# Kernel tuning notes

Hardware: AMD Instinct MI355X
Metric: run time of the kernel (lower is better)

Reference implementation:

```python
import jax, jax.numpy as jnp
import numpy as np

D_MODEL = 1024
N_HEADS = 16
D_HEAD = D_MODEL // N_HEADS
WINDOW = 256
SCALE = D_HEAD ** -0.5


def setup_inputs() -> dict:
    key = jax.random.key(0)
    k1, k2, k3, k4, k5 = jax.random.split(key, 5)
    B, S = 2, 2048
    x = jax.random.normal(k1, (B, S, D_MODEL), dtype=jnp.float32)
    s = 0.02
    Wqkv = jax.random.normal(k2, (D_MODEL, 3 * D_MODEL), dtype=jnp.float32) * s
    bqkv = jnp.zeros((3 * D_MODEL,), dtype=jnp.float32)
    Wout = jax.random.normal(k3, (D_MODEL, D_MODEL), dtype=jnp.float32) * s
    bout = jnp.zeros((D_MODEL,), dtype=jnp.float32)
    return {"x": x, "Wqkv": Wqkv, "bqkv": bqkv, "Wout": Wout, "bout": bout}


def reference(x, Wqkv, bqkv, Wout, bout):
    B, S, D = x.shape
    qkv = x @ Wqkv + bqkv                       # (B, S, 3D)
    q, k, v = jnp.split(qkv, 3, axis=-1)
    # (B, H, S, d)
    q = q.reshape(B, S, N_HEADS, D_HEAD).transpose(0, 2, 1, 3)
    k = k.reshape(B, S, N_HEADS, D_HEAD).transpose(0, 2, 1, 3)
    v = v.reshape(B, S, N_HEADS, D_HEAD).transpose(0, 2, 1, 3)
    scores = jnp.einsum('bhqd,bhkd->bhqk', q, k) * SCALE
    # windowed causal mask: allow j <= i and j >= i - WINDOW (inclusive),
    # matching torch code where mask[i, :i-window_size] = 0 for i >= window_size
    i = jnp.arange(S)[:, None]
    j = jnp.arange(S)[None, :]
    allowed = (j <= i) & (j >= i - WINDOW)      # (S, S)
    scores = jnp.where(allowed[None, None], scores, -jnp.inf)
    attn = jax.nn.softmax(scores, axis=-1)      # dropout=0 / eval mode
    out = jnp.einsum('bhqk,bhkd->bhqd', attn, v)
    out = out.transpose(0, 2, 1, 3).reshape(B, S, D)
    return out @ Wout + bout
```

## Files before the change

kernel.cpp:

```cpp
#include <hip/hip_runtime.h>
#include <stdint.h>


typedef __attribute__((ext_vector_type(8))) short bf16x8;
typedef __attribute__((ext_vector_type(4))) float f32x4;
typedef __attribute__((ext_vector_type(4))) unsigned int u32x4;
typedef __attribute__((ext_vector_type(4))) unsigned short u16x4;

#define DEV static __device__ __forceinline__

#define SC2 0.18033688011112042f

DEV unsigned short f2bf(float f) {
  unsigned int u = __builtin_bit_cast(unsigned int, f);
  u += 0x7fffu + ((u >> 16) & 1u);
  return (unsigned short)(u >> 16);
}

DEV void gload_lds16(const void* g, void* l) {
  __builtin_amdgcn_global_load_lds((const __attribute__((address_space(1))) void*)g,
                                   (__attribute__((address_space(3))) void*)l,
                                   16, 0, 0);
}

__global__ __launch_bounds__(256) void k_prep(const float* __restrict__ x,
                                              const float* __restrict__ Wqkv,
                                              const float* __restrict__ Wout,
                                              const float* __restrict__ bqkv,
                                              unsigned short* __restrict__ xb,
                                              unsigned short* __restrict__ wqT,
                                              unsigned short* __restrict__ woT,
                                              float* __restrict__ bqkv_s) {
  __shared__ float t[32][33];
  const int bid = blockIdx.x, tid = threadIdx.x;
  if (bid < 4096) {
    int i = bid * 256 + tid;
    f32x4 v = ((const f32x4*)x)[i];
    u16x4 o;
    o[0] = f2bf(v[0]); o[1] = f2bf(v[1]); o[2] = f2bf(v[2]); o[3] = f2bf(v[3]);
    ((u16x4*)xb)[i] = o;
    return;
  }
  if (bid >= 8192) {
    int i = (bid - 8192) * 256 + tid;
    if (i < 3072) bqkv_s[i] = bqkv[i] * (i < 1024 ? SC2 : 1.0f);
    return;
  }
  const float* in;
  unsigned short* out;
  int N, K, n0, k0;
  float wscale = 1.0f;
  if (bid < 7168) {
    int tt = bid - 4096;
    in = Wqkv; out = wqT; N = 3072; K = 1024;
    n0 = (tt % 96) * 32; k0 = (tt / 96) * 32;
    if (n0 < 1024) wscale = SC2;
  } else {
    int tt = bid - 7168;
    in = Wout; out = woT; N = 1024; K = 1024;
    n0 = (tt % 32) * 32; k0 = (tt / 32) * 32;
  }
  const int tx = tid & 31, ty = tid >> 5;
#pragma unroll
  for (int i = 0; i < 4; ++i)
    t[ty + i * 8][tx] = in[(size_t)(k0 + ty + i * 8) * N + n0 + tx];
  __syncthreads();
#pragma unroll
  for (int i = 0; i < 4; ++i)
    out[(size_t)(n0 + ty + i * 8) * K + k0 + tx] = f2bf(t[tx][ty + i * 8] * wscale);
}

template <int BN, bool F32OUT, bool FUSE_VT>
__global__ __launch_bounds__(512) void k_gemmbig(const unsigned short* __restrict__ A,
                                                 const unsigned short* __restrict__ Bt,
                                                 const float* __restrict__ bias,
                                                 void* __restrict__ Cout,
                                                 unsigned short* __restrict__ vT,
                                                 int M, int N, int K) {
  constexpr int NI = BN / 32;
  constexpr int ACH = 32;
  constexpr int NCH = ACH + BN / 8;
  constexpr int ASZ = 256 * 64;
  constexpr int BSZ = BN * 64;
  extern __shared__ unsigned short lds[];
  const int tid = threadIdx.x;
  const int lane = tid & 63, wid = tid >> 6;
  const int wr = wid >> 1, wc = wid & 1;
  const int g = lane >> 4, li = lane & 15;
  const int m0 = blockIdx.y * 256, n0 = blockIdx.x * BN;

  f32x4 acc[4][NI] = {};
  const int nkt = K >> 6;
  const int r8 = lane >> 3, sp = lane & 7;

  auto Abuf = [&](int i) { return lds + i * ASZ; };
  auto Bbuf = [&](int i) { return lds + 2 * ASZ + i * BSZ; };

  auto stage = [&](int bufi, int kt) {
#pragma unroll
    for (int c = wid; c < NCH; c += 8) {
      if (c < ACH) {
        int row = c * 8 + r8;
        int sl = sp ^ (row & 7);
        gload_lds16(A + (size_t)(m0 + row) * K + kt * 64 + sl * 8,
                    Abuf(bufi) + c * 512);
      } else {
        int cc = c - ACH;
        int row = cc * 8 + r8;
        int sl = sp ^ (row & 7);
        gload_lds16(Bt + (size_t)(n0 + row) * K + kt * 64 + sl * 8,
                    Bbuf(bufi) + cc * 512);
      }
    }
  };

  stage(0, 0);
  for (int kt = 0; kt < nkt; ++kt) {
    __syncthreads();
    if (kt + 1 < nkt) stage((kt + 1) & 1, kt + 1);
    const unsigned short* Ac = Abuf(kt & 1);
    const unsigned short* Bc = Bbuf(kt & 1);
#pragma unroll
    for (int h = 0; h < 2; ++h) {
      bf16x8 af[4], bfr[NI];
#pragma unroll
      for (int mi = 0; mi < 4; ++mi) {
        const int r = wr * 64 + mi * 16 + li;
        const int slot = (g + h * 4) ^ (r & 7);
        af[mi] = *(const bf16x8*)&Ac[r * 64 + slot * 8];
      }
#pragma unroll
      for (int ni = 0; ni < NI; ++ni) {
        const int r = wc * (BN / 2) + ni * 16 + li;
        const int slot = (g + h * 4) ^ (r & 7);
        bfr[ni] = *(const bf16x8*)&Bc[r * 64 + slot * 8];
      }
#pragma unroll
      for (int mi = 0; mi < 4; ++mi)
#pragma unroll
        for (int ni = 0; ni < NI; ++ni)
          acc[mi][ni] = __builtin_amdgcn_mfma_f32_16x16x32_bf16(af[mi], bfr[ni],
                                                                acc[mi][ni], 0, 0, 0);
    }
  }

  float bv[NI];
#pragma unroll
  for (int ni = 0; ni < NI; ++ni) bv[ni] = bias[n0 + wc * (BN / 2) + ni * 16 + li];
#pragma unroll
  for (int mi = 0; mi < 4; ++mi) {
#pragma unroll
    for (int ni = 0; ni < NI; ++ni) {
      const int col = n0 + wc * (BN / 2) + ni * 16 + li;
      const int row0 = m0 + wr * 64 + mi * 16 + g * 4;
      float v0 = acc[mi][ni][0] + bv[ni];
      float v1 = acc[mi][ni][1] + bv[ni];
      float v2 = acc[mi][ni][2] + bv[ni];
      float v3 = acc[mi][ni][3] + bv[ni];
      if (F32OUT) {
        float* C = (float*)Cout;
        C[(size_t)(row0 + 0) * N + col] = v0;
        C[(size_t)(row0 + 1) * N + col] = v1;
        C[(size_t)(row0 + 2) * N + col] = v2;
        C[(size_t)(row0 + 3) * N + col] = v3;
      } else {
        unsigned short* C = (unsigned short*)Cout;
        C[(size_t)(row0 + 0) * N + col] = f2bf(v0);
        C[(size_t)(row0 + 1) * N + col] = f2bf(v1);
        C[(size_t)(row0 + 2) * N + col] = f2bf(v2);
        C[(size_t)(row0 + 3) * N + col] = f2bf(v3);
      }
      if (FUSE_VT && col >= 2048) {
        const int b = row0 >> 11;
        const int s = row0 & 2047;
        u16x4 vv;
        vv[0] = f2bf(v0); vv[1] = f2bf(v1); vv[2] = f2bf(v2); vv[3] = f2bf(v3);
        *(u16x4*)&vT[(size_t)(b * 1024 + col - 2048) * 2048 + s] = vv;
      }
    }
  }
}

__global__ __launch_bounds__(256) void k_attn3(const unsigned short* __restrict__ qkv,
                                               const unsigned short* __restrict__ vT,
                                               unsigned short* __restrict__ attn) {
  __shared__ unsigned short Ks[2][64 * 64];
  __shared__ unsigned short Vs[2][64 * 64];
  __shared__ unsigned short Ps[64 * 88];
  const int tid = threadIdx.x, lane = tid & 63, wid = tid >> 6;
  const int g = lane >> 4, li = lane & 15;
  const int bh = blockIdx.y, b = bh >> 4, h = bh & 15;
  const int q0 = blockIdx.x * 64;
  const size_t rs = 3072;
  const unsigned short* qb = qkv + (size_t)b * 2048 * rs + h * 64;
  const unsigned short* kb = qb + 1024;
  const unsigned short* vb = vT + (size_t)bh * 64 * 2048;

  const int qrow = wid * 16 + li;
  const bf16x8 qf0 = *(const bf16x8*)(qb + (size_t)(q0 + qrow) * rs + (g << 3));
  const bf16x8 qf1 = *(const bf16x8*)(qb + (size_t)(q0 + qrow) * rs + 32 + (g << 3));

  const int tf = (blockIdx.x >= 4) ? 0 : (4 - (int)blockIdx.x);

  auto stage = [&](int bufi, int t) {
    const int j0 = q0 - 256 + t * 64;
    const int sl = (lane & 7) ^ ((lane >> 3) & 7);
#pragma unroll
    for (int j = 0; j < 2; ++j) {
      const int chunk = wid * 2 + j;
      const int row = chunk * 8 + (lane >> 3);
      gload_lds16(kb + (size_t)(j0 + row) * rs + sl * 8, &Ks[bufi][chunk * 512]);
      gload_lds16(vb + (size_t)row * 2048 + j0 + sl * 8, &Vs[bufi][chunk * 512]);
    }
  };

  f32x4 o[4] = {};
  float l_part[4] = {0.f, 0.f, 0.f, 0.f};

  stage(0, tf);
  int cur = 0;
  for (int t = tf; t < 5; ++t) {
    if (t + 1 < 5) {
      stage(cur ^ 1, t + 1);
      asm volatile("s_waitcnt vmcnt(4)" ::: "memory");
    } else {
      asm volatile("s_waitcnt vmcnt(0)" ::: "memory");
    }
    __builtin_amdgcn_sched_barrier(0);
    __builtin_amdgcn_s_barrier();
    __builtin_amdgcn_sched_barrier(0);

    const unsigned short* Kc = Ks[cur];
    const unsigned short* Vc = Vs[cur];

    f32x4 s[4];
#pragma unroll
    for (int ni = 0; ni < 4; ++ni) {
      const int kr = ni * 16 + li;
      const int sw = (kr & 7);
      bf16x8 kf0 = *(const bf16x8*)&Kc[kr * 64 + ((g ^ sw) << 3)];
      bf16x8 kf1 = *(const bf16x8*)&Kc[kr * 64 + (((4 + g) ^ sw) << 3)];
      f32x4 z = {};
      z = __builtin_amdgcn_mfma_f32_16x16x32_bf16(qf0, kf0, z, 0, 0, 0);
      z = __builtin_amdgcn_mfma_f32_16x16x32_bf16(qf1, kf1, z, 0, 0, 0);
      s[ni] = z;
    }
    const int rt = wid * 16 + g * 4;
#pragma unroll
    for (int ni = 0; ni < 4; ++ni) {
      int ct = ni * 16 + li;
#pragma unroll
      for (int reg = 0; reg < 4; ++reg) {
        float sv = s[ni][reg];
        if (t == 4 && ct > rt + reg) sv = -3e30f;
        if (t == 0 && ct < rt + reg) sv = -3e30f;
        s[ni][reg] = sv;
      }
    }
#pragma unroll
    for (int reg = 0; reg < 4; ++reg) {
      float ps = 0.f;
#pragma unroll
      for (int ni = 0; ni < 4; ++ni) {
        float p = __builtin_exp2f(s[ni][reg] - 16.0f);
        ps += p;
        Ps[(wid * 16 + g * 4 + reg) * 88 + ni * 16 + li] = f2bf(p);
      }
      l_part[reg] += ps;
    }
    asm volatile("s_waitcnt lgkmcnt(0)" ::: "memory");
    __builtin_amdgcn_sched_barrier(0);
    const bf16x8 pf0 = *(const bf16x8*)&Ps[(wid * 16 + li) * 88 + (g << 3)];
    const bf16x8 pf1 = *(const bf16x8*)&Ps[(wid * 16 + li) * 88 + 32 + (g << 3)];
#pragma unroll
    for (int ni = 0; ni < 4; ++ni) {
      const int dr = ni * 16 + li;
      const int sw = (dr & 7);
      bf16x8 vf0 = *(const bf16x8*)&Vc[dr * 64 + ((g ^ sw) << 3)];
      bf16x8 vf1 = *(const bf16x8*)&Vc[dr * 64 + (((4 + g) ^ sw) << 3)];
      o[ni] = __builtin_amdgcn_mfma_f32_16x16x32_bf16(pf0, vf0, o[ni], 0, 0, 0);
      o[ni] = __builtin_amdgcn_mfma_f32_16x16x32_bf16(pf1, vf1, o[ni], 0, 0, 0);
    }
    __builtin_amdgcn_sched_barrier(0);
    __builtin_amdgcn_s_barrier();
    cur ^= 1;
  }

  float inv[4];
#pragma unroll
  for (int reg = 0; reg < 4; ++reg) {
    float L = l_part[reg];
    L += __shfl_xor(L, 1, 64);
    L += __shfl_xor(L, 2, 64);
    L += __shfl_xor(L, 4, 64);
    L += __shfl_xor(L, 8, 64);
    inv[reg] = 1.f / L;
  }
#pragma unroll
  for (int ni = 0; ni < 4; ++ni) {
#pragma unroll
    for (int reg = 0; reg < 4; ++reg) {
      size_t row = (size_t)b * 2048 + q0 + wid * 16 + g * 4 + reg;
      attn[row * 1024 + h * 64 + ni * 16 + li] = f2bf(o[ni][reg] * inv[reg]);
    }
  }
}

extern "C" void kernel_launch(void* const* d_in, const int* in_sizes, int n_in,
                              void* d_out, int out_size, void* d_ws, size_t ws_size,
                              hipStream_t stream) {
  const float* x    = (const float*)d_in[0];
  const float* Wqkv = (const float*)d_in[1];
  const float* bqkv = (const float*)d_in[2];
  const float* Wout = (const float*)d_in[3];
  const float* bout = (const float*)d_in[4];
  float* out = (float*)d_out;

  uint8_t* ws = (uint8_t*)d_ws;
  unsigned short* xb    = (unsigned short*)(ws);
  unsigned short* wqT   = (unsigned short*)(ws +  8388608);
  unsigned short* woT   = (unsigned short*)(ws + 14680064);
  unsigned short* qkvb  = (unsigned short*)(ws + 16777216);
  unsigned short* attnb = (unsigned short*)(ws + 41943040);
  unsigned short* vTb   = (unsigned short*)(ws + 50331648);
  float*          bqs   = (float*)(ws + 58720256);

  hipFuncSetAttribute((const void*)k_gemmbig<192, false, true>,
                      hipFuncAttributeMaxDynamicSharedMemorySize, 114688);
  hipFuncSetAttribute((const void*)k_gemmbig<64, true, false>,
                      hipFuncAttributeMaxDynamicSharedMemorySize, 81920);

  k_prep<<<8204, 256, 0, stream>>>(x, Wqkv, Wout, bqkv, xb, wqT, woT, bqs);
  k_gemmbig<192, false, true><<<dim3(3072 / 192, 4096 / 256), 512, 114688, stream>>>(
      xb, wqT, bqs, qkvb, vTb, 4096, 3072, 1024);
  k_attn3<<<dim3(2048 / 64, 32), 256, 0, stream>>>(qkvb, vTb, attnb);
  k_gemmbig<64, true, false><<<dim3(1024 / 64, 4096 / 256), 512, 81920, stream>>>(
      attnb, woT, bout, out, nullptr, 4096, 1024, 1024);
}
```

Measured before the change: 85.73 us.

## Double attention query tile to 128 rows with 8 waves sharing K/V tiles

The windowed attention kernel now handles 128 query rows per block with 512 threads. The two 4-wave halves share each staged 64-row K/V tile, and each half skips the one tile outside its window. This roughly cuts K/V global loads and staging per query row while giving each thread fewer staging loads. The cost is half the number of blocks, an extra tile iteration per block where some waves idle at barriers, and a larger LDS footprint for P.

```diff
diff --git a/kernel.cpp b/kernel.cpp
--- a/kernel.cpp
+++ b/kernel.cpp
@@ -181,16 +181,16 @@
   }
 }
 
-__global__ __launch_bounds__(256) void k_attn3(const unsigned short* __restrict__ qkv,
+__global__ __launch_bounds__(512) void k_attn5(const unsigned short* __restrict__ qkv,
                                                const unsigned short* __restrict__ vT,
                                                unsigned short* __restrict__ attn) {
   __shared__ unsigned short Ks[2][64 * 64];
   __shared__ unsigned short Vs[2][64 * 64];
-  __shared__ unsigned short Ps[64 * 88];
+  __shared__ unsigned short Ps[128 * 88];
   const int tid = threadIdx.x, lane = tid & 63, wid = tid >> 6;
   const int g = lane >> 4, li = lane & 15;
   const int bh = blockIdx.y, b = bh >> 4, h = bh & 15;
-  const int q0 = blockIdx.x * 64;
+  const int bx = blockIdx.x, q0 = bx * 128;
   const size_t rs = 3072;
   const unsigned short* qb = qkv + (size_t)b * 2048 * rs + h * 64;
   const unsigned short* kb = qb + 1024;
@@ -200,29 +200,27 @@
   const bf16x8 qf0 = *(const bf16x8*)(qb + (size_t)(q0 + qrow) * rs + (g << 3));
   const bf16x8 qf1 = *(const bf16x8*)(qb + (size_t)(q0 + qrow) * rs + 32 + (g << 3));
 
-  const int tf = (blockIdx.x >= 4) ? 0 : (4 - (int)blockIdx.x);
+  const int tf_blk = (bx >= 2) ? 0 : (4 - 2 * bx);
+  const int tfw = (wid >= 4) ? 1 : 0;
+  const int tlw = tfw + 4;
 
   auto stage = [&](int bufi, int t) {
     const int j0 = q0 - 256 + t * 64;
-    const int sl = (lane & 7) ^ ((lane >> 3) & 7);
-#pragma unroll
-    for (int j = 0; j < 2; ++j) {
-      const int chunk = wid * 2 + j;
-      const int row = chunk * 8 + (lane >> 3);
-      gload_lds16(kb + (size_t)(j0 + row) * rs + sl * 8, &Ks[bufi][chunk * 512]);
-      gload_lds16(vb + (size_t)row * 2048 + j0 + sl * 8, &Vs[bufi][chunk * 512]);
-    }
+    const int row = wid * 8 + (lane >> 3);
+    const int sl = (lane & 7) ^ (row & 7);
+    gload_lds16(kb + (size_t)(j0 + row) * rs + sl * 8, &Ks[bufi][wid * 512]);
+    gload_lds16(vb + (size_t)row * 2048 + j0 + sl * 8, &Vs[bufi][wid * 512]);
   };
 
   f32x4 o[4] = {};
   float l_part[4] = {0.f, 0.f, 0.f, 0.f};
 
-  stage(0, tf);
+  stage(0, tf_blk);
   int cur = 0;
-  for (int t = tf; t < 5; ++t) {
-    if (t + 1 < 5) {
+  for (int t = tf_blk; t < 6; ++t) {
+    if (t + 1 < 6) {
       stage(cur ^ 1, t + 1);
-      asm volatile("s_waitcnt vmcnt(4)" ::: "memory");
+      asm volatile("s_waitcnt vmcnt(2)" ::: "memory");
     } else {
       asm volatile("s_waitcnt vmcnt(0)" ::: "memory");
     }
@@ -230,56 +228,58 @@
     __builtin_amdgcn_s_barrier();
     __builtin_amdgcn_sched_barrier(0);
 
-    const unsigned short* Kc = Ks[cur];
-    const unsigned short* Vc = Vs[cur];
-
-    f32x4 s[4];
-#pragma unroll
-    for (int ni = 0; ni < 4; ++ni) {
-      const int kr = ni * 16 + li;
-      const int sw = (kr & 7);
-      bf16x8 kf0 = *(const bf16x8*)&Kc[kr * 64 + ((g ^ sw) << 3)];
-      bf16x8 kf1 = *(const bf16x8*)&Kc[kr * 64 + (((4 + g) ^ sw) << 3)];
-      f32x4 z = {};
-      z = __builtin_amdgcn_mfma_f32_16x16x32_bf16(qf0, kf0, z, 0, 0, 0);
-      z = __builtin_amdgcn_mfma_f32_16x16x32_bf16(qf1, kf1, z, 0, 0, 0);
-      s[ni] = z;
-    }
-    const int rt = wid * 16 + g * 4;
-#pragma unroll
-    for (int ni = 0; ni < 4; ++ni) {
-      int ct = ni * 16 + li;
+    if (t >= tfw && t <= tlw) {
+      const unsigned short* Kc = Ks[cur];
+      const unsigned short* Vc = Vs[cur];
+
+      f32x4 s[4];
+#pragma unroll
+      for (int ni = 0; ni < 4; ++ni) {
+        const int kr = ni * 16 + li;
+        const int sw = (kr & 7);
+        bf16x8 kf0 = *(const bf16x8*)&Kc[kr * 64 + ((g ^ sw) << 3)];
+        bf16x8 kf1 = *(const bf16x8*)&Kc[kr * 64 + (((4 + g) ^ sw) << 3)];
+        f32x4 z = {};
+        z = __builtin_amdgcn_mfma_f32_16x16x32_bf16(qf0, kf0, z, 0, 0, 0);
+        z = __builtin_amdgcn_mfma_f32_16x16x32_bf16(qf1, kf1, z, 0, 0, 0);
+        s[ni] = z;
+      }
+      const int rt = (wid & 3) * 16 + g * 4;
+#pragma unroll
+      for (int ni = 0; ni < 4; ++ni) {
+        int ct = ni * 16 + li;
+#pragma unroll
+        for (int reg = 0; reg < 4; ++reg) {
+          float sv = s[ni][reg];
+          if (t == tlw && ct > rt + reg) sv = -3e30f;
+          if (t == tfw && ct < rt + reg) sv = -3e30f;
+          s[ni][reg] = sv;
+        }
+      }
 #pragma unroll
       for (int reg = 0; reg < 4; ++reg) {
-        float sv = s[ni][reg];
-        if (t == 4 && ct > rt + reg) sv = -3e30f;
-        if (t == 0 && ct < rt + reg) sv = -3e30f;
-        s[ni][reg] = sv;
-      }
-    }
-#pragma unroll
-    for (int reg = 0; reg < 4; ++reg) {
-      float ps = 0.f;
+        float ps = 0.f;
+#pragma unroll
+        for (int ni = 0; ni < 4; ++ni) {
+          float p = __builtin_exp2f(s[ni][reg] - 16.0f);
+          ps += p;
+          Ps[(wid * 16 + g * 4 + reg) * 88 + ni * 16 + li] = f2bf(p);
+        }
+        l_part[reg] += ps;
+      }
+      asm volatile("s_waitcnt lgkmcnt(0)" ::: "memory");
+      __builtin_amdgcn_sched_barrier(0);
+      const bf16x8 pf0 = *(const bf16x8*)&Ps[(wid * 16 + li) * 88 + (g << 3)];
+      const bf16x8 pf1 = *(const bf16x8*)&Ps[(wid * 16 + li) * 88 + 32 + (g << 3)];
 #pragma unroll
       for (int ni = 0; ni < 4; ++ni) {
-        float p = __builtin_exp2f(s[ni][reg] - 16.0f);
-        ps += p;
-        Ps[(wid * 16 + g * 4 + reg) * 88 + ni * 16 + li] = f2bf(p);
-      }
-      l_part[reg] += ps;
-    }
-    asm volatile("s_waitcnt lgkmcnt(0)" ::: "memory");
-    __builtin_amdgcn_sched_barrier(0);
-    const bf16x8 pf0 = *(const bf16x8*)&Ps[(wid * 16 + li) * 88 + (g << 3)];
-    const bf16x8 pf1 = *(const bf16x8*)&Ps[(wid * 16 + li) * 88 + 32 + (g << 3)];
-#pragma unroll
-    for (int ni = 0; ni < 4; ++ni) {
-      const int dr = ni * 16 + li;
-      const int sw = (dr & 7);
-      bf16x8 vf0 = *(const bf16x8*)&Vc[dr * 64 + ((g ^ sw) << 3)];
-      bf16x8 vf1 = *(const bf16x8*)&Vc[dr * 64 + (((4 + g) ^ sw) << 3)];
-      o[ni] = __builtin_amdgcn_mfma_f32_16x16x32_bf16(pf0, vf0, o[ni], 0, 0, 0);
-      o[ni] = __builtin_amdgcn_mfma_f32_16x16x32_bf16(pf1, vf1, o[ni], 0, 0, 0);
+        const int dr = ni * 16 + li;
+        const int sw = (dr & 7);
+        bf16x8 vf0 = *(const bf16x8*)&Vc[dr * 64 + ((g ^ sw) << 3)];
+        bf16x8 vf1 = *(const bf16x8*)&Vc[dr * 64 + (((4 + g) ^ sw) << 3)];
+        o[ni] = __builtin_amdgcn_mfma_f32_16x16x32_bf16(pf0, vf0, o[ni], 0, 0, 0);
+        o[ni] = __builtin_amdgcn_mfma_f32_16x16x32_bf16(pf1, vf1, o[ni], 0, 0, 0);
+      }
     }
     __builtin_amdgcn_sched_barrier(0);
     __builtin_amdgcn_s_barrier();
@@ -333,7 +333,7 @@
   k_prep<<<8204, 256, 0, stream>>>(x, Wqkv, Wout, bqkv, xb, wqT, woT, bqs);
   k_gemmbig<192, false, true><<<dim3(3072 / 192, 4096 / 256), 512, 114688, stream>>>(
       xb, wqT, bqs, qkvb, vTb, 4096, 3072, 1024);
-  k_attn3<<<dim3(2048 / 64, 32), 256, 0, stream>>>(qkvb, vTb, attnb);
+  k_attn5<<<dim3(2048 / 128, 32), 512, 0, stream>>>(qkvb, vTb, attnb);
   k_gemmbig<64, true, false><<<dim3(1024 / 64, 4096 / 256), 512, 81920, stream>>>(
       attnb, woT, bout, out, nullptr, 4096, 1024, 1024);
 }
```

After: 81.21 us. 5.3% less time.
